# Kernel tuning notes

Measured on AMD Instinct MI355X. Metric: run time of the kernel, lower is better.

Reference implementation:

```python
import jax, jax.numpy as jnp
import numpy as np

GRID = 32
N = GRID * GRID
KTOP = 256          # max off-diagonal points kept per diagram (rest are diagonal, zero cost)
SINK_ITERS = 150
_idx = np.arange(N).reshape(GRID, GRID)
_EU = np.concatenate([_idx[:, :-1].ravel(), _idx[:-1, :].ravel()]).astype(np.int32)
_EV = np.concatenate([_idx[:, 1:].ravel(), _idx[1:, :].ravel()]).astype(np.int32)
E = _EU.shape[0]  # 1984 grid edges (4-connectivity, V-construction cubical complex)


def _h0_pairs(v):
    """0-dim persistence pairs of the sublevel filtration of pixel values v [N].
    Kruskal/union-find with the elder rule; trivial edges emit diagonal (w, w) pairs."""
    eu, ev = jnp.asarray(_EU), jnp.asarray(_EV)
    w = jnp.maximum(v[eu], v[ev])
    order = jnp.argsort(w)

    @jax.checkpoint
    def step(state, edge):
        parent, birth = state
        u, vv, wgt = edge
        for _ in range(10):              # pointer jumping: full compression (2^10 >= N)
            parent = parent[parent]
        ru, rv = parent[u], parent[vv]
        bu, bv = birth[ru], birth[rv]
        merge = ru != rv
        u_older = bu <= bv
        older = jnp.where(u_older, ru, rv)
        younger = jnp.where(u_older, rv, ru)
        pb = jnp.where(merge, jnp.maximum(bu, bv), wgt)   # younger component dies
        parent = parent.at[younger].set(jnp.where(merge, older, younger))
        birth = birth.at[older].set(jnp.minimum(bu, bv))
        return (parent, birth), (pb, wgt)

    init = (jnp.arange(N, dtype=jnp.int32), v)
    _, (bs, ds) = jax.lax.scan(step, init, (eu[order], ev[order], w[order]))
    return bs, ds


def _diagrams(img):
    """img [GRID,GRID] -> (b0, d0, b1, d1), each [KTOP]. H1 via superlevel H0 duality."""
    v = img.reshape(-1)
    b0, d0 = _h0_pairs(v)
    b0 = jnp.concatenate([b0, v.min()[None]])   # essential H0 class: (min, max)
    d0 = jnp.concatenate([d0, v.max()[None]])
    nb, nd = _h0_pairs(-v)                       # superlevel-set H0 (essential dropped)
    b1, d1 = -nd, -nb

    def topk(b, d):
        _, i = jax.lax.top_k(d - b, KTOP)        # keep most persistent points
        return b[i], d[i]

    return (*topk(b0, d0), *topk(b1, d1))


def _wasserstein(ab, ad, bb, bd):
    """Entropic 1-Wasserstein between diagrams with L-inf ground metric and diagonal slots."""
    K = ab.shape[0]
    Pa = jnp.stack([ab, ad], -1)
    Pb = jnp.stack([bb, bd], -1)
    Mpp = jnp.max(jnp.abs(Pa[:, None, :] - Pb[None, :, :]), -1)  # [K,K]
    da = 0.5 * (ad - ab)                       # L-inf distance of a-points to diagonal
    db = 0.5 * (bd - bb)
    C = jnp.block([[Mpp, jnp.broadcast_to(da[:, None], (K, K))],
                   [jnp.broadcast_to(db[None, :], (K, K)), jnp.zeros((K, K), ab.dtype)]])
    eps = 0.02 * jnp.maximum(jnp.max(C), 1e-6)

    def it(_, fg):
        f, g = fg
        f = -eps * jax.nn.logsumexp((g[None, :] - C) / eps, axis=1)
        g = -eps * jax.nn.logsumexp((f[:, None] - C) / eps, axis=0)
        return f, g

    f, g = jax.lax.fori_loop(0, SINK_ITERS, it, (jnp.zeros(2 * K), jnp.zeros(2 * K)))
    P = jnp.exp((f[:, None] + g[None, :] - C) / eps)
    return jnp.sum(P * C)


def setup_inputs() -> dict:
    key = jax.random.key(0)
    kx, ky = jax.random.split(key)
    x = jax.random.normal(kx, (4, 4, 256, 256), dtype=jnp.float32)
    y = jax.random.randint(ky, (4, 1, 256, 256), 0, 4)
    return {"x": x, "y": y}


def reference(x, y):
    B, C, H, W = x.shape
    x = jax.nn.softmax(x, axis=1)                               # apply_nonlin
    y_oh = (y == jnp.arange(C)[None, :, None, None]).astype(x.dtype)  # scatter_ one-hot
    kh, kw = H // GRID, W // GRID

    def pool(t):  # adaptive_avg_pool2d to (32, 32)
        b, c = t.shape[:2]
        return t.reshape(b, c, GRID, kh, GRID, kw).mean((3, 5))

    mx = pool(x[:, 1:]).reshape(-1, GRID, GRID)  # drop background channel
    my = pool(y_oh[:, 1:]).reshape(-1, GRID, GRID)
    dx = jax.vmap(_diagrams)(mx)
    dy = jax.vmap(_diagrams)(my)
    w0 = jax.vmap(_wasserstein)(dx[0], dx[1], dy[0], dy[1])
    w1 = jax.vmap(_wasserstein)(dx[2], dx[3], dy[2], dy[3])
    return (jnp.sum(w0) + jnp.sum(w1)) / B
```

## Files before the change

kernel.cpp:

```cpp
#include <hip/hip_runtime.h>
#include <cmath>

#define NPIX 1024
#define NEDGE 1984
#define NPAD 2048
#define KTOP 256
#define NITER 150

typedef __attribute__((ext_vector_type(8))) short bf16x8_t;
typedef __attribute__((ext_vector_type(4))) float f32x4_t;

__device__ __forceinline__ unsigned bf_rne(float x) {
    unsigned b = __float_as_uint(x);
    return (b + 0x7fffu + ((b >> 16) & 1u)) >> 16;
}
__device__ __forceinline__ float rcpf(float x) { return __builtin_amdgcn_rcpf(x); }

template<int CTRL>
__device__ __forceinline__ float dppf(float x) {
    return __int_as_float(__builtin_amdgcn_update_dpp(
        __float_as_int(x), __float_as_int(x), CTRL, 0xF, 0xF, false));
}
__device__ __forceinline__ void wave_red2(float& s, float& m) {
    s += dppf<0x121>(s); m = fminf(m, dppf<0x121>(m));
    s += dppf<0x122>(s); m = fminf(m, dppf<0x122>(m));
    s += dppf<0x124>(s); m = fminf(m, dppf<0x124>(m));
    s += dppf<0x128>(s); m = fminf(m, dppf<0x128>(m));
    s += __int_as_float(__builtin_amdgcn_ds_swizzle(__float_as_int(s), 0x401F));
    m = fminf(m, __int_as_float(__builtin_amdgcn_ds_swizzle(__float_as_int(m), 0x401F)));
    float s0 = __int_as_float(__builtin_amdgcn_readlane(__float_as_int(s), 0));
    float s1 = __int_as_float(__builtin_amdgcn_readlane(__float_as_int(s), 32));
    s = s0 + s1;
    float m0 = __int_as_float(__builtin_amdgcn_readlane(__float_as_int(m), 0));
    float m1 = __int_as_float(__builtin_amdgcn_readlane(__float_as_int(m), 32));
    m = fminf(m0, m1);
}

__device__ __forceinline__ float min8v(const float* a) {
    float4 x0 = *(const float4*)a, x1 = *(const float4*)(a + 4);
    return fminf(fminf(fminf(x0.x, x0.y), fminf(x0.z, x0.w)),
                 fminf(fminf(x1.x, x1.y), fminf(x1.z, x1.w)));
}
__device__ __forceinline__ float sum8v(const float* a) {
    float4 x0 = *(const float4*)a, x1 = *(const float4*)(a + 4);
    return ((x0.x + x0.y) + (x0.z + x0.w)) + ((x1.x + x1.y) + (x1.z + x1.w));
}

__global__ __launch_bounds__(256) void pool_kernel(const float* __restrict__ x,
                                                   const int* __restrict__ y,
                                                   float* __restrict__ pooled) {
    int blk = blockIdx.x;
    int img = blk >> 2;
    int cell = ((blk & 3) << 8) | threadIdx.x;
    int gi = cell >> 5, gj = cell & 31;
    const float L2E = 1.4426950408889634f;
    float acc = 0.f;
    if (img < 12) {
        int b = img / 3, c = img % 3 + 1;
        const float* xb = x + (size_t)b * 262144 + (size_t)gi * 2048 + gj * 8;
        for (int pi = 0; pi < 8; ++pi) {
            const float* xr = xb + pi * 256;
            #pragma unroll
            for (int ph = 0; ph < 2; ++ph) {
                float4 c0 = *(const float4*)(xr + ph * 4);
                float4 c1 = *(const float4*)(xr + ph * 4 + 65536);
                float4 c2 = *(const float4*)(xr + ph * 4 + 131072);
                float4 c3 = *(const float4*)(xr + ph * 4 + 196608);
                const float* f0 = (const float*)&c0;
                const float* f1 = (const float*)&c1;
                const float* f2 = (const float*)&c2;
                const float* f3 = (const float*)&c3;
                #pragma unroll
                for (int k = 0; k < 4; ++k) {
                    float e0 = exp2f(f0[k] * L2E), e1 = exp2f(f1[k] * L2E);
                    float e2 = exp2f(f2[k] * L2E), e3 = exp2f(f3[k] * L2E);
                    float ec = (c == 1) ? e1 : (c == 2) ? e2 : e3;
                    acc += ec / (e0 + e1 + e2 + e3);
                }
            }
        }
    } else {
        int tt = img - 12;
        int b = tt / 3, c = tt % 3 + 1;
        const int* yb = y + (size_t)b * 65536 + (size_t)gi * 2048 + gj * 8;
        int cnt = 0;
        for (int pi = 0; pi < 8; ++pi) {
            const int* yr = yb + pi * 256;
            #pragma unroll
            for (int pj = 0; pj < 8; ++pj) cnt += (yr[pj] == c) ? 1 : 0;
        }
        acc = (float)cnt;
    }
    pooled[img * NPIX + cell] = acc * (1.f / 64.f);
}

__device__ void bitonic2048(unsigned long long* keys, int tid, bool asc) {
    for (int k = 2; k <= NPAD; k <<= 1) {
        for (int j = k >> 1; j > 0; j >>= 1) {
            for (int ii = tid; ii < NPAD; ii += 512) {
                int l = ii ^ j;
                if (l > ii) {
                    unsigned long long a = keys[ii], b = keys[l];
                    bool up = (((ii & k) == 0) == asc);
                    if ((a > b) == up) { keys[ii] = b; keys[l] = a; }
                }
            }
            __syncthreads();
        }
    }
}

__global__ __launch_bounds__(512) void diag_kernel(const float* __restrict__ pooled,
                                                   float* __restrict__ diag) {
    __shared__ float v_[NPIX];
    __shared__ unsigned long long keys[NPAD];
    __shared__ unsigned long long PB[NPIX];
    __shared__ unsigned euv[NPAD];
    __shared__ unsigned long long pbd[NEDGE];
    __shared__ float redA[8], redB[8];
    __shared__ float svmin, svmax;

    int run = blockIdx.x;
    int img = run >> 1, filt = run & 1;
    int tid = threadIdx.x;
    const float* m = pooled + img * NPIX;

    for (int i = tid; i < NPIX; i += 512) {
        float val = m[i];
        v_[i] = filt ? -val : val;
    }
    __syncthreads();
    float mn = INFINITY, mx = -INFINITY;
    for (int i = tid; i < NPIX; i += 512) { float vv = v_[i]; mn = fminf(mn, vv); mx = fmaxf(mx, vv); }
    for (int o = 32; o; o >>= 1) { mn = fminf(mn, __shfl_xor(mn, o)); mx = fmaxf(mx, __shfl_xor(mx, o)); }
    if ((tid & 63) == 0) { redA[tid >> 6] = mn; redB[tid >> 6] = mx; }
    __syncthreads();
    if (tid == 0) {
        float a = INFINITY, b = -INFINITY;
        for (int i2 = 0; i2 < 8; ++i2) { a = fminf(a, redA[i2]); b = fmaxf(b, redB[i2]); }
        svmin = a; svmax = b;
    }
    for (int e = tid; e < NPAD; e += 512) {
        unsigned long long key;
        unsigned uv = 0;
        if (e < NEDGE) {
            int u, vv;
            if (e < 992) { int r = e / 31; u = e + r; vv = u + 1; }
            else         { u = e - 992;   vv = u + 32; }
            float w = fmaxf(v_[u], v_[vv]);
            unsigned int bw = __float_as_uint(w);
            bw = (bw & 0x80000000u) ? ~bw : (bw | 0x80000000u);
            key = ((unsigned long long)bw << 11) | (unsigned int)e;
            uv = (unsigned)u | ((unsigned)vv << 16);
        } else key = ~0ULL;
        keys[e] = key;
        euv[e] = uv;
    }
    for (int i = tid; i < NPIX; i += 512)
        PB[i] = ((unsigned long long)__float_as_uint(v_[i]) << 32) | (unsigned)i;
    __syncthreads();
    bitonic2048(keys, tid, true);

    unsigned* PBlo = (unsigned*)PB;
    for (int base = 0; base < NEDGE; base += 128) {
        if (base) {
            for (int rd = 0; rd < 4; ++rd) {
                for (int i = tid; i < NPIX; i += 512) {
                    unsigned pp = PBlo[2 * i];
                    unsigned gg = PBlo[2 * pp];
                    PBlo[2 * i] = gg;
                }
            }
        }
        __syncthreads();
        if (tid == 0) {
            int bend = (base + 128 < NEDGE) ? base + 128 : NEDGE;
            unsigned long long kc = keys[base];
            unsigned long long kn = keys[base + 1];
            unsigned uvc = euv[(int)(kc & 2047ULL)];
            for (int kk = base; kk < bend; ++kk) {
                unsigned long long k2 = keys[kk + 2];
                unsigned uvn = euv[(int)(kn & 2047ULL)];
                unsigned ob = (unsigned)(kc >> 11);
                float w = __uint_as_float((ob & 0x80000000u) ? (ob & 0x7fffffffu) : ~ob);
                int u = (int)(uvc & 0xffffu), vv = (int)(uvc >> 16);
                int a = u, b = vv;
                unsigned long long qa = PB[a], qb = PB[b];
                int pa = (int)(unsigned)qa, pb = (int)(unsigned)qb;
                while (pa != a || pb != b) {
                    if (pa != a) {
                        unsigned long long na = PB[pa];
                        int ga = (int)(unsigned)na;
                        PBlo[2 * a] = (unsigned)ga;
                        a = pa; pa = ga; qa = na;
                    }
                    if (pb != b) {
                        unsigned long long nb = PB[pb];
                        int gb = (int)(unsigned)nb;
                        PBlo[2 * b] = (unsigned)gb;
                        b = pb; pb = gb; qb = nb;
                    }
                }
                float pb_, pd_;
                if (a != b) {
                    float bu = __uint_as_float((unsigned)(qa >> 32));
                    float bv = __uint_as_float((unsigned)(qb >> 32));
                    bool uo = (bu <= bv);
                    int older = uo ? a : b;
                    int younger = uo ? b : a;
                    pb_ = fmaxf(bu, bv); pd_ = w;
                    PBlo[2 * younger] = (unsigned)older;
                } else { pb_ = w; pd_ = w; }
                pbd[kk] = (unsigned long long)__float_as_uint(pb_)
                        | ((unsigned long long)__float_as_uint(pd_) << 32);
                kc = kn; kn = k2; uvc = uvn;
            }
        }
        __syncthreads();
    }

    int count = filt ? NEDGE : (NEDGE + 1);
    for (int k = tid; k < NPAD; k += 512) {
        unsigned long long key = 0ULL;
        if (k < count) {
            float pers;
            if (k < NEDGE) {
                unsigned long long pd2 = pbd[k];
                pers = __uint_as_float((unsigned)(pd2 >> 32)) - __uint_as_float((unsigned)pd2);
            } else pers = svmax - svmin;
            key = ((unsigned long long)__float_as_uint(pers) << 32) | (unsigned int)(2047 - k);
        }
        keys[k] = key;
    }
    __syncthreads();
    bitonic2048(keys, tid, false);

    if (tid < KTOP) {
        unsigned long long key = keys[tid];
        int k = 2047 - (int)(key & 0xffffffffULL);
        float b_, d_;
        if (k < NEDGE) {
            unsigned long long pd2 = pbd[k];
            b_ = __uint_as_float((unsigned)pd2);
            d_ = __uint_as_float((unsigned)(pd2 >> 32));
        } else { b_ = svmin; d_ = svmax; }
        float ob, od;
        if (!filt) { ob = b_;  od = d_;  }
        else       { ob = -d_; od = -b_; }
        diag[((img * 4) + filt * 2 + 0) * KTOP + tid] = ob;
        diag[((img * 4) + filt * 2 + 1) * KTOP + tid] = od;
    }
}

__global__ __launch_bounds__(512) void sink_kernel(const float* __restrict__ diag,
                                                   float* __restrict__ wres) {
    __shared__ float2 sPA[KTOP], sPB[KTOP];
    __shared__ float sda[KTOP], sdb[KTOP];
    __shared__ float swa[KTOP], swb[KTOP];
    __shared__ __align__(16) unsigned ug_bf[128];
    __shared__ __align__(16) unsigned uf_bf[128];
    __shared__ __align__(16) float uf32[KTOP], ug32[KTOP];
    __shared__ __align__(16) float minF[8], accTF[8], minG[8], accTG[8];
    __shared__ __align__(16) float pm[8];
    __shared__ float s_sig, s_invsig;

    int p = blockIdx.x;
    int img = p % 12, dim = p / 12;
    int t = threadIdx.x;
    int lane = t & 63, w = t >> 6;
    int lr = lane & 15, lg = lane >> 4;
    int r = t >> 1, q = t & 1, jb = q * 128;

    const float* ab  = diag + ((img * 4) + dim * 2) * KTOP;
    const float* ad  = ab + KTOP;
    const float* bbp = diag + (((12 + img) * 4) + dim * 2) * KTOP;
    const float* bdp = bbp + KTOP;

    if (t < KTOP) {
        float a0 = ab[t], a1 = ad[t];
        float b0 = bbp[t], b1 = bdp[t];
        sPA[t] = make_float2(a0, a1);
        sPB[t] = make_float2(b0, b1);
        sda[t] = 0.5f * (a1 - a0);
        sdb[t] = 0.5f * (b1 - b0);
    }
    if (t < 128) ug_bf[t] = 0x3F803F80u;
    __syncthreads();

    {
        float2 A = sPA[r];
        float lmax = 0.f;
        for (int jj = 0; jj < 128; ++jj) {
            float2 B = sPB[jb + jj];
            lmax = fmaxf(lmax, fmaxf(fabsf(A.x - B.x), fabsf(A.y - B.y)));
        }
        if (t < KTOP) lmax = fmaxf(lmax, fmaxf(sda[t], sdb[t]));
        for (int o = 32; o; o >>= 1) lmax = fmaxf(lmax, __shfl_xor(lmax, o));
        if (lane == 0) pm[w] = lmax;
    }
    __syncthreads();
    if (t == 0) {
        float mc = 0.f;
        for (int i = 0; i < 8; ++i) mc = fmaxf(mc, pm[i]);
        float eps = 0.02f * fmaxf(mc, 1e-6f);
        s_sig = 1.4426950408889634f / eps;
        s_invsig = eps * 0.6931471805599453f;
    }
    __syncthreads();
    {
        float sig = s_sig;
        if (t < KTOP) {
            float2 a2 = sPA[t], b2 = sPB[t];
            sPA[t] = make_float2(a2.x * sig, a2.y * sig);
            sPB[t] = make_float2(b2.x * sig, b2.y * sig);
            float da2 = sda[t] * sig, db2 = sdb[t] * sig;
            sda[t] = da2; sdb[t] = db2;
            swa[t] = exp2f(-da2); swb[t] = exp2f(-db2);
        }
    }
    __syncthreads();

    bf16x8_t KfA0[8], KfA1[8], KgA0[8], KgA1[8];
    {
        float2 Af0 = sPA[w * 32 + lr];
        float2 Af1 = sPA[w * 32 + 16 + lr];
        float2 Bg0 = sPB[w * 32 + lr];
        float2 Bg1 = sPB[w * 32 + 16 + lr];
        #pragma unroll
        for (int ks = 0; ks < 8; ++ks) {
            #pragma unroll
            for (int jj = 0; jj < 8; ++jj) {
                int b = ks * 32 + lg * 8 + jj;
                float2 Pb = sPB[b];
                KfA0[ks][jj] = (short)bf_rne(exp2f(-fmaxf(fabsf(Af0.x - Pb.x), fabsf(Af0.y - Pb.y))));
                KfA1[ks][jj] = (short)bf_rne(exp2f(-fmaxf(fabsf(Af1.x - Pb.x), fabsf(Af1.y - Pb.y))));
                float2 Pa = sPA[b];
                KgA0[ks][jj] = (short)bf_rne(exp2f(-fmaxf(fabsf(Pa.x - Bg0.x), fabsf(Pa.y - Bg0.y))));
                KgA1[ks][jj] = (short)bf_rne(exp2f(-fmaxf(fabsf(Pa.x - Bg1.x), fabsf(Pa.y - Bg1.y))));
            }
        }
    }
    float wa0[4], wa1[4], wb0[4], wb1[4];
    #pragma unroll
    for (int g2 = 0; g2 < 4; ++g2) {
        wa0[g2] = swa[w * 32 + lg * 4 + g2];
        wa1[g2] = swa[w * 32 + 16 + lg * 4 + g2];
        wb0[g2] = swb[w * 32 + lg * 4 + g2];
        wb1[g2] = swb[w * 32 + 16 + lg * 4 + g2];
    }

    float cg = 1.f, cf = 1.f, uG2s = 1.f, uF2s = 1.f;
    f32x4_t ugs0 = {1.f, 1.f, 1.f, 1.f}, ugs1 = {1.f, 1.f, 1.f, 1.f};
    f32x4_t ufs0 = {0.f, 0.f, 0.f, 0.f}, ufs1 = {0.f, 0.f, 0.f, 0.f};

    for (int it = 0; it < NITER; ++it) {
        if (it) {
            cg = min8v(minG);
            uG2s = rcpf(cf * (sum8v(accTG) + 256.f * uF2s));
        }
        {
            bf16x8_t Bf[8];
            #pragma unroll
            for (int ks = 0; ks < 8; ++ks) Bf[ks] = ((const bf16x8_t*)ug_bf)[ks * 4 + lg];
            f32x4_t a0 = {0.f, 0.f, 0.f, 0.f}, a1 = {0.f, 0.f, 0.f, 0.f};
            #pragma unroll
            for (int ks = 0; ks < 8; ++ks) {
                a0 = __builtin_amdgcn_mfma_f32_16x16x32_bf16(KfA0[ks], Bf[ks], a0, 0, 0, 0);
                a1 = __builtin_amdgcn_mfma_f32_16x16x32_bf16(KfA1[ks], Bf[ks], a1, 0, 0, 0);
            }
            float mv = INFINITY, tv = 0.f;
            #pragma unroll
            for (int g2 = 0; g2 < 4; ++g2) {
                float R0 = cg * (a0[g2] + 256.f * uG2s * wa0[g2]);
                float R1 = cg * (a1[g2] + 256.f * uG2s * wa1[g2]);
                ufs0[g2] = rcpf(R0); ufs1[g2] = rcpf(R1);
                mv = fminf(mv, fminf(R0, R1));
                tv += ugs0[g2] * wb0[g2] + ugs1[g2] * wb1[g2];
            }
            if (lr == 0) {
                uint2 v0, v1;
                v0.x = bf_rne(ufs0[0]) | (bf_rne(ufs0[1]) << 16);
                v0.y = bf_rne(ufs0[2]) | (bf_rne(ufs0[3]) << 16);
                v1.x = bf_rne(ufs1[0]) | (bf_rne(ufs1[1]) << 16);
                v1.y = bf_rne(ufs1[2]) | (bf_rne(ufs1[3]) << 16);
                ((uint2*)uf_bf)[w * 8 + lg] = v0;
                ((uint2*)uf_bf)[w * 8 + 4 + lg] = v1;
            }
            wave_red2(tv, mv);
            if (lane == 0) { accTF[w] = tv * 0.0625f; minF[w] = mv; }
        }
        __syncthreads();
        cf = min8v(minF);
        uF2s = rcpf(cg * (sum8v(accTF) + 256.f * uG2s));
        {
            bf16x8_t Bf[8];
            #pragma unroll
            for (int ks = 0; ks < 8; ++ks) Bf[ks] = ((const bf16x8_t*)uf_bf)[ks * 4 + lg];
            f32x4_t a0 = {0.f, 0.f, 0.f, 0.f}, a1 = {0.f, 0.f, 0.f, 0.f};
            #pragma unroll
            for (int ks = 0; ks < 8; ++ks) {
                a0 = __builtin_amdgcn_mfma_f32_16x16x32_bf16(KgA0[ks], Bf[ks], a0, 0, 0, 0);
                a1 = __builtin_amdgcn_mfma_f32_16x16x32_bf16(KgA1[ks], Bf[ks], a1, 0, 0, 0);
            }
            float mv = INFINITY, tv = 0.f;
            #pragma unroll
            for (int g2 = 0; g2 < 4; ++g2) {
                float Q0 = cf * (a0[g2] + 256.f * uF2s * wb0[g2]);
                float Q1 = cf * (a1[g2] + 256.f * uF2s * wb1[g2]);
                ugs0[g2] = rcpf(Q0); ugs1[g2] = rcpf(Q1);
                mv = fminf(mv, fminf(Q0, Q1));
                tv += ufs0[g2] * wa0[g2] + ufs1[g2] * wa1[g2];
            }
            if (lr == 0) {
                uint2 v0, v1;
                v0.x = bf_rne(ugs0[0]) | (bf_rne(ugs0[1]) << 16);
                v0.y = bf_rne(ugs0[2]) | (bf_rne(ugs0[3]) << 16);
                v1.x = bf_rne(ugs1[0]) | (bf_rne(ugs1[1]) << 16);
                v1.y = bf_rne(ugs1[2]) | (bf_rne(ugs1[3]) << 16);
                ((uint2*)ug_bf)[w * 8 + lg] = v0;
                ((uint2*)ug_bf)[w * 8 + 4 + lg] = v1;
            }
            wave_red2(tv, mv);
            if (lane == 0) { accTG[w] = tv * 0.0625f; minG[w] = mv; }
        }
        __syncthreads();
    }
    float uG2f = rcpf(cf * (sum8v(accTG) + 256.f * uF2s));
    if (lr == 0) {
        ((f32x4_t*)uf32)[w * 8 + lg] = ufs0;
        ((f32x4_t*)uf32)[w * 8 + 4 + lg] = ufs1;
        ((f32x4_t*)ug32)[w * 8 + lg] = ugs0;
        ((f32x4_t*)ug32)[w * 8 + 4 + lg] = ugs1;
    }
    __syncthreads();

    float accv = 0.f;
    {
        float2 Apt = sPA[r];
        float ufr = uf32[r];
        #pragma unroll 8
        for (int jj = 0; jj < 128; ++jj) {
            int j = jb + jj;
            float2 B = sPB[j];
            float Mh = fmaxf(fabsf(Apt.x - B.x), fabsf(Apt.y - B.y));
            float kv = __uint_as_float(bf_rne(exp2f(-Mh)) << 16);
            accv += ((ufr * kv) * ug32[j]) * Mh;
        }
        if (q == 0) accv += 256.f * ((ufr * swa[r]) * uG2f) * sda[r];
        else        accv += 256.f * ((uF2s * swb[r]) * ug32[r]) * sdb[r];
    }
    accv *= cf;
    for (int o = 32; o; o >>= 1) accv += __shfl_xor(accv, o);
    if (lane == 0) pm[w] = accv;
    __syncthreads();
    if (t == 0) {
        float tot = 0.f;
        for (int i = 0; i < 8; ++i) tot += pm[i];
        wres[p] = tot * s_invsig;
    }
}

__global__ void finalize_kernel(const float* __restrict__ wres, float* __restrict__ out) {
    if (threadIdx.x == 0) {
        float s = 0.f;
        for (int i = 0; i < 24; ++i) s += wres[i];
        out[0] = s * 0.25f;
    }
}

extern "C" void kernel_launch(void* const* d_in, const int* in_sizes, int n_in,
                              void* d_out, int out_size, void* d_ws, size_t ws_size,
                              hipStream_t stream) {
    const float* x = (const float*)d_in[0];
    const int* y = (const int*)d_in[1];
    float* ws = (float*)d_ws;
    float* pooled = ws;
    float* diag = pooled + 24 * NPIX;
    float* wres = diag + 24 * 4 * KTOP;

    pool_kernel<<<96, 256, 0, stream>>>(x, y, pooled);
    diag_kernel<<<48, 512, 0, stream>>>(pooled, diag);
    sink_kernel<<<24, 512, 0, stream>>>(diag, wres);
    finalize_kernel<<<1, 64, 0, stream>>>(wres, (float*)d_out);
}
```

Measured before the change: 910.0 us.

## Parallel pre-filter of edges already connected at batch start before serial union-find

Before the single-thread Kruskal loop for each batch of 128 edges, one thread per edge finds the roots of both endpoints against the batch-start forest. Edges whose endpoints already share a root are written out directly as diagonal pairs. The remaining edges are packed into a shared snapshot array with their pre-resolved roots, so the serial thread skips trivial edges and starts its find from roots rather than raw endpoints. This shortens the serial critical path, at the cost of an extra parallel phase and barrier per batch. The snap array is read one entry past the batch end, and that slot may hold stale data from an earlier batch.

```diff
diff --git a/kernel.cpp b/kernel.cpp
--- a/kernel.cpp
+++ b/kernel.cpp
@@ -117,6 +117,7 @@
     __shared__ unsigned long long PB[NPIX];
     __shared__ unsigned euv[NPAD];
     __shared__ unsigned long long pbd[NEDGE];
+    __shared__ unsigned long long snap[132];
     __shared__ float redA[8], redB[8];
     __shared__ float svmin, svmax;
 
@@ -173,47 +174,68 @@
             }
         }
         __syncthreads();
+        int bend = (base + 128 < NEDGE) ? base + 128 : NEDGE;
+        int bcnt = bend - base;
+        if (tid < bcnt) {
+            int kk = base + tid;
+            unsigned long long key = keys[kk];
+            int e = (int)(key & 2047ULL);
+            unsigned bw = (unsigned)(key >> 11);
+            unsigned uv = euv[e];
+            int ra = (int)(uv & 0xffffu), rb = (int)(uv >> 16);
+            unsigned pp = PBlo[2 * ra];
+            while (pp != (unsigned)ra) { ra = (int)pp; pp = PBlo[2 * ra]; }
+            unsigned p2 = PBlo[2 * rb];
+            while (p2 != (unsigned)rb) { rb = (int)p2; p2 = PBlo[2 * rb]; }
+            if (ra == rb) {
+                unsigned wb = (bw & 0x80000000u) ? (bw & 0x7fffffffu) : ~bw;
+                pbd[kk] = (unsigned long long)wb | ((unsigned long long)wb << 32);
+                snap[tid] = (unsigned long long)bw << 22;
+            } else {
+                snap[tid] = ((unsigned long long)bw << 22)
+                          | ((unsigned)(ra + 1) << 11) | (unsigned)(rb + 1);
+            }
+        }
+        __syncthreads();
         if (tid == 0) {
-            int bend = (base + 128 < NEDGE) ? base + 128 : NEDGE;
-            unsigned long long kc = keys[base];
-            unsigned long long kn = keys[base + 1];
-            unsigned uvc = euv[(int)(kc & 2047ULL)];
-            for (int kk = base; kk < bend; ++kk) {
-                unsigned long long k2 = keys[kk + 2];
-                unsigned uvn = euv[(int)(kn & 2047ULL)];
-                unsigned ob = (unsigned)(kc >> 11);
-                float w = __uint_as_float((ob & 0x80000000u) ? (ob & 0x7fffffffu) : ~ob);
-                int u = (int)(uvc & 0xffffu), vv = (int)(uvc >> 16);
-                int a = u, b = vv;
-                unsigned long long qa = PB[a], qb = PB[b];
-                int pa = (int)(unsigned)qa, pb = (int)(unsigned)qb;
-                while (pa != a || pb != b) {
-                    if (pa != a) {
-                        unsigned long long na = PB[pa];
-                        int ga = (int)(unsigned)na;
-                        PBlo[2 * a] = (unsigned)ga;
-                        a = pa; pa = ga; qa = na;
+            unsigned long long sc = snap[0];
+            for (int i = 0; i < bcnt; ++i) {
+                unsigned long long sn = snap[i + 1];
+                if ((unsigned)(sc & 0x3FFFFFu)) {
+                    unsigned ob = (unsigned)(sc >> 22);
+                    float w = __uint_as_float((ob & 0x80000000u) ? (ob & 0x7fffffffu) : ~ob);
+                    int a = (int)((sc >> 11) & 0x7FFu) - 1;
+                    int b = (int)(sc & 0x7FFu) - 1;
+                    unsigned long long qa = PB[a], qb = PB[b];
+                    int pa = (int)(unsigned)qa, pb = (int)(unsigned)qb;
+                    while (pa != a || pb != b) {
+                        if (pa != a) {
+                            unsigned long long na = PB[pa];
+                            int ga = (int)(unsigned)na;
+                            PBlo[2 * a] = (unsigned)ga;
+                            a = pa; pa = ga; qa = na;
+                        }
+                        if (pb != b) {
+                            unsigned long long nb = PB[pb];
+                            int gb = (int)(unsigned)nb;
+                            PBlo[2 * b] = (unsigned)gb;
+                            b = pb; pb = gb; qb = nb;
+                        }
                     }
-                    if (pb != b) {
-                        unsigned long long nb = PB[pb];
-                        int gb = (int)(unsigned)nb;
-                        PBlo[2 * b] = (unsigned)gb;
-                        b = pb; pb = gb; qb = nb;
-                    }
+                    float pb_, pd_;
+                    if (a != b) {
+                        float bu = __uint_as_float((unsigned)(qa >> 32));
+                        float bv = __uint_as_float((unsigned)(qb >> 32));
+                        bool uo = (bu <= bv);
+                        int older = uo ? a : b;
+                        int younger = uo ? b : a;
+                        pb_ = fmaxf(bu, bv); pd_ = w;
+                        PBlo[2 * younger] = (unsigned)older;
+                    } else { pb_ = w; pd_ = w; }
+                    pbd[base + i] = (unsigned long long)__float_as_uint(pb_)
+                                  | ((unsigned long long)__float_as_uint(pd_) << 32);
                 }
-                float pb_, pd_;
-                if (a != b) {
-                    float bu = __uint_as_float((unsigned)(qa >> 32));
-                    float bv = __uint_as_float((unsigned)(qb >> 32));
-                    bool uo = (bu <= bv);
-                    int older = uo ? a : b;
-                    int younger = uo ? b : a;
-                    pb_ = fmaxf(bu, bv); pd_ = w;
-                    PBlo[2 * younger] = (unsigned)older;
-                } else { pb_ = w; pd_ = w; }
-                pbd[kk] = (unsigned long long)__float_as_uint(pb_)
-                        | ((unsigned long long)__float_as_uint(pd_) << 32);
-                kc = kn; kn = k2; uvc = uvn;
+                sc = sn;
             }
         }
         __syncthreads();
```

Measured after the change: 892.9 us. About the same (-1.9%).
